# Performance work log

Measured on AMD Instinct MI355X. Metric: run time of the kernel, lower is better.

## Reference

```python
import jax, jax.numpy as jnp
import numpy as np

N_NODES = 25000
N_EDGES = 100000
N_GRAPHS = 1000
DIM = 64
NUM_FEAT = 14
EDGE_FEAT = 4
HIDDEN_EDGE = 128
NUM_OUT = 1
NUM_CONV_STEPS = 3
SET2SET_STEPS = 3
NEG_SLOPE = 0.01


def leaky_relu(x):
    return jnp.where(x > 0, x, NEG_SLOPE * x)


def setup_inputs() -> dict:
    key = jax.random.key(0)
    ks = jax.random.split(key, 24)
    s = lambda fan_in: 1.0 / np.sqrt(fan_in)
    inp = {
        "x": jax.random.normal(ks[0], (N_NODES, NUM_FEAT), dtype=jnp.float32),
        "edge_index": jax.random.randint(ks[1], (2, N_EDGES), 0, N_NODES),
        "edge_attr": jax.random.uniform(ks[2], (N_EDGES, EDGE_FEAT), dtype=jnp.float32),
        "batch": jnp.sort(jax.random.randint(ks[3], (N_NODES,), 0, N_GRAPHS)),
        # lin0
        "lin0_w": jax.random.normal(ks[4], (DIM, NUM_FEAT), dtype=jnp.float32) * s(NUM_FEAT),
        "lin0_b": jnp.zeros((DIM,), dtype=jnp.float32),
        # edge-weight MLP: Linear(4,128) -> LeakyReLU -> Linear(128, DIM*DIM)
        "net_w1": jax.random.normal(ks[5], (HIDDEN_EDGE, EDGE_FEAT), dtype=jnp.float32) * s(EDGE_FEAT),
        "net_b1": jnp.zeros((HIDDEN_EDGE,), dtype=jnp.float32),
        "net_w2": jax.random.normal(ks[6], (DIM * DIM, HIDDEN_EDGE), dtype=jnp.float32) * s(HIDDEN_EDGE),
        "net_b2": jnp.zeros((DIM * DIM,), dtype=jnp.float32),
        # NNConv root weight + bias
        "conv_root": jax.random.normal(ks[7], (DIM, DIM), dtype=jnp.float32) * s(DIM),
        "conv_bias": jnp.zeros((DIM,), dtype=jnp.float32),
        # GRU (single layer), torch gate order r,z,n
        "gru_w_ih": jax.random.normal(ks[8], (3 * DIM, DIM), dtype=jnp.float32) * s(DIM),
        "gru_w_hh": jax.random.normal(ks[9], (3 * DIM, DIM), dtype=jnp.float32) * s(DIM),
        "gru_b_ih": jnp.zeros((3 * DIM,), dtype=jnp.float32),
        "gru_b_hh": jnp.zeros((3 * DIM,), dtype=jnp.float32),
        # Set2Set LSTM: input 2*DIM -> hidden DIM, torch gate order i,f,g,o
        "lstm_w_ih": jax.random.normal(ks[10], (4 * DIM, 2 * DIM), dtype=jnp.float32) * s(2 * DIM),
        "lstm_w_hh": jax.random.normal(ks[11], (4 * DIM, DIM), dtype=jnp.float32) * s(DIM),
        "lstm_b_ih": jnp.zeros((4 * DIM,), dtype=jnp.float32),
        "lstm_b_hh": jnp.zeros((4 * DIM,), dtype=jnp.float32),
        # final linear on [B, 2*DIM]
        "lin_w": jax.random.normal(ks[12], (NUM_OUT, 2 * DIM), dtype=jnp.float32) * s(2 * DIM),
        "lin_b": jnp.zeros((NUM_OUT,), dtype=jnp.float32),
    }
    return inp


def _forward(x, edge_index, edge_attr, batch,
             lin0_w, lin0_b, net_w1, net_b1, net_w2, net_b2,
             conv_root, conv_bias, gru_w_ih, gru_w_hh, gru_b_ih, gru_b_hh,
             lstm_w_ih, lstm_w_hh, lstm_b_ih, lstm_b_hh, lin_w, lin_b):
    src, dst = edge_index[0], edge_index[1]

    out = leaky_relu(x @ lin0_w.T + lin0_b)          # [N, DIM]
    h = out                                          # GRU hidden [N, DIM]

    # edge_attr is constant across conv steps -> dynamic weights computed once
    W_e = (leaky_relu(edge_attr @ net_w1.T + net_b1) @ net_w2.T + net_b2)
    W_e = W_e.reshape(N_EDGES, DIM, DIM)             # [E, DIM, DIM]

    deg = jax.ops.segment_sum(jnp.ones((N_EDGES,), dtype=x.dtype), dst,
                              num_segments=N_NODES)
    inv_deg = jnp.where(deg > 0, 1.0 / jnp.maximum(deg, 1.0), 0.0)[:, None]

    for _ in range(NUM_CONV_STEPS):
        # NNConv: gather -> per-edge matmul -> scatter-mean, plus root term
        msg = jnp.einsum('ed,edo->eo', out[src], W_e)                 # [E, DIM]
        aggr = jax.ops.segment_sum(msg, dst, num_segments=N_NODES) * inv_deg
        m = leaky_relu(aggr + out @ conv_root + conv_bias)
        # single-step GRU (torch equations, gate order r,z,n)
        gi = m @ gru_w_ih.T + gru_b_ih
        gh = h @ gru_w_hh.T + gru_b_hh
        i_r, i_z, i_n = jnp.split(gi, 3, axis=-1)
        h_r, h_z, h_n = jnp.split(gh, 3, axis=-1)
        r = jax.nn.sigmoid(i_r + h_r)
        z = jax.nn.sigmoid(i_z + h_z)
        n = jnp.tanh(i_n + r * h_n)
        h = (1.0 - z) * n + z * h
        out = h

    # Set2Set pooling (processing_steps=3)
    q_star = jnp.zeros((N_GRAPHS, 2 * DIM), dtype=x.dtype)
    hl = jnp.zeros((N_GRAPHS, DIM), dtype=x.dtype)
    cl = jnp.zeros((N_GRAPHS, DIM), dtype=x.dtype)
    for _ in range(SET2SET_STEPS):
        gates = q_star @ lstm_w_ih.T + lstm_b_ih + hl @ lstm_w_hh.T + lstm_b_hh
        gi, gf, gg, go = jnp.split(gates, 4, axis=-1)
        cl = jax.nn.sigmoid(gf) * cl + jax.nn.sigmoid(gi) * jnp.tanh(gg)
        hl = jax.nn.sigmoid(go) * jnp.tanh(cl)
        q = hl                                                         # [B, DIM]
        e = jnp.sum(out * q[batch], axis=-1)                           # [N]
        e_max = jax.ops.segment_max(e, batch, num_segments=N_GRAPHS)
        e_exp = jnp.exp(e - e_max[batch])
        denom = jax.ops.segment_sum(e_exp, batch, num_segments=N_GRAPHS)
        a = e_exp / denom[batch]                                       # segment softmax
        r_read = jax.ops.segment_sum(a[:, None] * out, batch,
                                     num_segments=N_GRAPHS)            # [B, DIM]
        q_star = jnp.concatenate([q, r_read], axis=-1)

    return q_star @ lin_w.T + lin_b                                    # [B, NUM_OUT]


def reference(x, edge_index, edge_attr, batch,
              lin0_w, lin0_b, net_w1, net_b1, net_w2, net_b2,
              conv_root, conv_bias, gru_w_ih, gru_w_hh, gru_b_ih, gru_b_hh,
              lstm_w_ih, lstm_w_hh, lstm_b_ih, lstm_b_hh, lin_w, lin_b):
    return _forward(x, edge_index, edge_attr, batch,
                    lin0_w, lin0_b, net_w1, net_b1, net_w2, net_b2,
                    conv_root, conv_bias, gru_w_ih, gru_w_hh, gru_b_ih, gru_b_hh,
                    lstm_w_ih, lstm_w_hh, lstm_b_ih, lstm_b_hh, lin_w, lin_b)
```

## Files before the change

### kernel.cpp

```cpp
#include <hip/hip_runtime.h>
#include <math.h>

#define N_NODES_C  25000
#define N_EDGES_C  100000
#define N_GRAPHS_C 1000
#define EPB 128

typedef __attribute__((ext_vector_type(8))) _Float16 f16x8;
typedef __attribute__((ext_vector_type(2))) _Float16 f16x2;
typedef __attribute__((ext_vector_type(4))) float   f32x4;

__device__ __forceinline__ float lrelu(float x) { return x > 0.f ? x : 0.01f * x; }
__device__ __forceinline__ float sigm(float x)  { return 1.f / (1.f + __expf(-x)); }
__device__ __forceinline__ f32x4 MFH(f16x8 a, f16x8 b, f32x4 c) {
  return __builtin_amdgcn_mfma_f32_16x16x32_f16(a, b, c, 0, 0, 0);
}

__global__ __launch_bounds__(256) void lin0_kernel(const float* __restrict__ x,
                            const float* __restrict__ w, const float* __restrict__ b,
                            float* __restrict__ nodeF) {
  __shared__ float ws[64 * 15];
  __shared__ float bs[64];
  __shared__ float xr[4][16];
  const int tid = threadIdx.x;
  for (int i = tid; i < 896; i += 256) { int o = i / 14, j = i % 14; ws[o * 15 + j] = w[i]; }
  if (tid < 64) bs[tid] = b[tid];
  const int nl = tid >> 6, o = tid & 63;
  const int n = blockIdx.x * 4 + nl;
  if (o < 14 && n < N_NODES_C) xr[nl][o] = x[n * 14 + o];
  __syncthreads();
  if (n < N_NODES_C) {
    float s = bs[o];
#pragma unroll
    for (int j = 0; j < 14; ++j) s += xr[nl][j] * ws[o * 15 + j];
    nodeF[n * 64 + o] = lrelu(s);
  }
}

__global__ void deg_kernel(const int* __restrict__ ei, const int* __restrict__ batch,
                           float* __restrict__ deg, int* __restrict__ goff) {
  int e = blockIdx.x * blockDim.x + threadIdx.x;
  if (e < N_EDGES_C) atomicAdd(&deg[ei[N_EDGES_C + e]], 1.f);
  if (e <= N_GRAPHS_C) {
    int lo = 0, hi = N_NODES_C;
    while (lo < hi) { int mid = (lo + hi) >> 1; if (batch[mid] < e) lo = mid + 1; else hi = mid; }
    goff[e] = lo;
  }
}

__global__ void invdeg_kernel(float* __restrict__ deg) {
  int n = blockIdx.x * blockDim.x + threadIdx.x;
  if (n < N_NODES_C) { float v = deg[n]; deg[n] = v > 0.f ? 1.f / v : 0.f; }
}

__global__ __launch_bounds__(256) void prep_kernel(
    const float* __restrict__ net_w2, const float* __restrict__ net_b2,
    const float* __restrict__ conv_root,
    const float* __restrict__ w_ih, const float* __restrict__ w_hh,
    _Float16* __restrict__ Wp, _Float16* __restrict__ B2p,
    _Float16* __restrict__ Rtp, _Float16* __restrict__ Wip, _Float16* __restrict__ Whp) {
  int i = blockIdx.x * 256 + threadIdx.x;
  {
    int j = i & 7, lane = (i >> 3) & 63, q = (i >> 9) & 3, p = (i >> 11) & 1;
    int oh = (i >> 12) & 1, d = i >> 13;
    int kci = q >> 1, ob = q & 1;
    int col = lane & 15, kg = lane >> 4;
    int o = oh * 32 + ob * 16 + col, h = (p * 2 + kci) * 32 + kg * 8 + j;
    Wp[i] = (_Float16)net_w2[((size_t)d * 64 + o) * 128 + h];
  }
  if (i < 4096) {
    int j = i & 7, lane = (i >> 3) & 63, kc2 = (i >> 9) & 1, ob = (i >> 10) & 1, oh = (i >> 11) & 1;
    int col = lane & 15, kg = lane >> 4;
    int o = oh * 32 + ob * 16 + col, d = kc2 * 32 + kg * 8 + j;
    B2p[i] = (_Float16)net_b2[d * 64 + o];
  }
  if (i < 12288) {
    int j = i & 7, lane = (i >> 3) & 63, kc = (i >> 9) & 1, t = i >> 10;
    int o = t * 16 + (lane & 15), d = kc * 32 + (lane >> 4) * 8 + j;
    if (i < 4096) Rtp[i] = (_Float16)conv_root[d * 64 + o];
    Wip[i] = (_Float16)w_ih[o * 64 + d];
    Whp[i] = (_Float16)w_hh[o * 64 + d];
  }
}

__global__ __launch_bounds__(256, 3) void msg_kernel(
    const float* __restrict__ nodef,
    const int*   __restrict__ ei,
    const float* __restrict__ eattr,
    const float* __restrict__ net_w1,
    const float* __restrict__ net_b1,
    const _Float16* __restrict__ Wp,
    const _Float16* __restrict__ B2p,
    float* __restrict__ aggr)
{
  __shared__ _Float16 xsT[EPB * 64];
  __shared__ float    w1s[128 * 5];

  const int tid = threadIdx.x;
  const int e0 = blockIdx.x * EPB;

  if (tid < 128) {
    float4 wv = *(const float4*)(net_w1 + tid * 4);
    w1s[tid * 5 + 0] = wv.x; w1s[tid * 5 + 1] = wv.y;
    w1s[tid * 5 + 2] = wv.z; w1s[tid * 5 + 3] = wv.w;
    w1s[tid * 5 + 4] = net_b1[tid];
  }
  {
    const int e = tid >> 1, dh = (tid & 1) * 32;
    int ge = e0 + e;
    const int esw = (e & 7) << 3;
#pragma unroll
    for (int jb = 0; jb < 4; ++jb) {
      int d = dh + jb * 8;
      float4 v0, v1;
      if (ge < N_EDGES_C) {
        const float4* nf4 = (const float4*)(nodef + (size_t)ei[ge] * 64 + d);
        v0 = nf4[0]; v1 = nf4[1];
      } else {
        v0 = make_float4(0.f, 0.f, 0.f, 0.f); v1 = v0;
      }
      f16x8 pk;
      pk[0] = (_Float16)v0.x; pk[1] = (_Float16)v0.y; pk[2] = (_Float16)v0.z; pk[3] = (_Float16)v0.w;
      pk[4] = (_Float16)v1.x; pk[5] = (_Float16)v1.y; pk[6] = (_Float16)v1.z; pk[7] = (_Float16)v1.w;
      *(f16x8*)&xsT[e * 64 + (d ^ esw)] = pk;
    }
  }

  const int lane = tid & 63, wv = tid >> 6;
  const int e0w = (wv & 1) * 64;
  const int oh  = wv >> 1;
  const int col = lane & 15;
  const int kg  = lane >> 4;
  const int swz = (col & 7) << 3;

  __syncthreads();

  f32x4 acc[4][2];
#pragma unroll
  for (int eb = 0; eb < 4; ++eb) { acc[eb][0] = 0.f; acc[eb][1] = 0.f; }
#pragma unroll
  for (int ob = 0; ob < 2; ++ob)
#pragma unroll
    for (int kc2 = 0; kc2 < 2; ++kc2) {
      f16x8 b2f = *(const f16x8*)(B2p + oh * 2048 + ob * 1024 + kc2 * 512 + lane * 8);
#pragma unroll
      for (int eb = 0; eb < 4; ++eb) {
        f16x8 xf = *(const f16x8*)&xsT[(e0w + eb * 16 + col) * 64 + ((kc2 * 32 + kg * 8) ^ swz)];
        acc[eb][ob] = MFH(xf, b2f, acc[eb][ob]);
      }
    }

  float4 at[4];
#pragma unroll
  for (int eb = 0; eb < 4; ++eb) {
    int ge = e0 + e0w + eb * 16 + col;
    at[eb] = (ge < N_EDGES_C) ? *(const float4*)(eattr + (size_t)ge * 4)
                              : make_float4(0.f, 0.f, 0.f, 0.f);
  }

#define ISSUE(BUF, ADDR)                                                  \
  asm volatile("global_load_dwordx4 %0, %4, off\n\t"                      \
               "global_load_dwordx4 %1, %4, off offset:1024\n\t"          \
               "global_load_dwordx4 %2, %4, off offset:2048\n\t"          \
               "global_load_dwordx4 %3, %4, off offset:3072"              \
               : "=&v"(BUF[0]), "=&v"(BUF[1]), "=&v"(BUF[2]), "=&v"(BUF[3]) \
               : "v"(ADDR)                                                \
               : "memory")
#define COMPUTE(BUF, XV, J)                                               \
  {                                                                       \
    _Pragma("unroll")                                                     \
    for (int eb = 0; eb < 4; ++eb) {                                      \
      unsigned dw = XV[eb].u[(J) >> 1];                                   \
      unsigned xd = __builtin_amdgcn_perm(dw, dw, ((J) & 1) ? 0x03020302u : 0x01000100u); \
      f16x2 x2; { union { unsigned u; f16x2 h; } c; c.u = xd; x2 = c.h; } \
      _Pragma("unroll")                                                   \
      for (int kci = 0; kci < 2; ++kci) {                                 \
        union { f16x8 v; f16x2 pp[4]; } af, Uu;                           \
        af.v = Af[eb][kci];                                               \
        _Pragma("unroll")                                                 \
        for (int q = 0; q < 4; ++q) Uu.pp[q] = af.pp[q] * x2;             \
        acc[eb][0] = MFH(Uu.v, BUF[kci * 2 + 0], acc[eb][0]);             \
        acc[eb][1] = MFH(Uu.v, BUF[kci * 2 + 1], acc[eb][1]);             \
      }                                                                   \
    }                                                                     \
  }

  const _Float16* wp_base = Wp + oh * 4096 + lane * 8;
#pragma unroll 1
  for (int p = 0; p < 2; ++p) {
    f16x8 Af[4][2];
#pragma unroll
    for (int kci = 0; kci < 2; ++kci) {
      float4 wr[8]; float wb[8];
#pragma unroll
      for (int j = 0; j < 8; ++j) {
        int hq = (p * 2 + kci) * 32 + kg * 8 + j;
        wr[j] = *(const float4*)&w1s[hq * 5];
        wb[j] = w1s[hq * 5 + 4];
      }
#pragma unroll
      for (int eb = 0; eb < 4; ++eb) {
        f16x8 F;
#pragma unroll
        for (int j = 0; j < 8; ++j) {
          float a = wb[j] + at[eb].x * wr[j].x + at[eb].y * wr[j].y
                          + at[eb].z * wr[j].z + at[eb].w * wr[j].w;
          F[j] = (_Float16)lrelu(a);
        }
        Af[eb][kci] = F;
      }
    }

    const _Float16* wp_p = wp_base + p * 2048;
    f16x8 B0[4], B1[4];
    ISSUE(B0, wp_p);
    ISSUE(B1, wp_p + 8192);

#pragma unroll 1
    for (int d8 = 0; d8 < 64; d8 += 8) {
      union XU { f16x8 v; unsigned u[4]; };
      XU XV[4];
#pragma unroll
      for (int eb = 0; eb < 4; ++eb)
        XV[eb].v = *(const f16x8*)&xsT[(e0w + eb * 16 + col) * 64 + (d8 ^ swz)];
#pragma unroll
      for (int j = 0; j < 8; ++j) {
        const int d = d8 + j;
        if (d < 63) { asm volatile("s_waitcnt vmcnt(4)"); }
        else        { asm volatile("s_waitcnt vmcnt(0)"); }
        __builtin_amdgcn_sched_barrier(0);
        if ((j & 1) == 0) { COMPUTE(B0, XV, j); } else { COMPUTE(B1, XV, j); }
        __builtin_amdgcn_sched_barrier(0);
        if (d < 62) {
          const _Float16* adr = wp_p + (size_t)(d + 2) * 8192;
          if ((j & 1) == 0) { ISSUE(B0, adr); } else { ISSUE(B1, adr); }
        }
      }
    }
  }
#undef ISSUE
#undef COMPUTE

  const int o0w = oh * 32;
#pragma unroll
  for (int eb = 0; eb < 4; ++eb) {
#pragma unroll
    for (int r = 0; r < 4; ++r) {
      int e = e0w + eb * 16 + kg * 4 + r;
      int ge = e0 + e;
      if (ge < N_EDGES_C) {
        int dn = ei[N_EDGES_C + ge];
        atomicAdd(&aggr[(size_t)dn * 64 + o0w + col],      acc[eb][0][r]);
        atomicAdd(&aggr[(size_t)dn * 64 + o0w + 16 + col], acc[eb][1][r]);
      }
    }
  }
}

__global__ __launch_bounds__(128) void node_update_kernel(
    float* __restrict__ aggr, const float* __restrict__ invdeg,
    const _Float16* __restrict__ Rtp, const _Float16* __restrict__ Wip,
    const _Float16* __restrict__ Whp,
    const float* __restrict__ conv_bias,
    const float* __restrict__ b_ih, const float* __restrict__ b_hh,
    float* __restrict__ nodeF)
{
  __shared__ _Float16 ms[2][16 * 64];

  const int tid = threadIdx.x, lane = tid & 63, wv = tid >> 6;
  const int col = lane & 15, kg = lane >> 4;
  const int nwb = blockIdx.x * 32 + wv * 16;

  float invd[4]; int nrow[4];
#pragma unroll
  for (int r = 0; r < 4; ++r) {
    int nn = nwb + kg * 4 + r; nrow[r] = nn;
    invd[r] = (nn < N_NODES_C) ? invdeg[nn] : 0.f;
  }
  float ag[4][4];
#pragma unroll
  for (int t = 0; t < 4; ++t)
#pragma unroll
    for (int r = 0; r < 4; ++r) {
      int nn = nrow[r];
      ag[t][r] = (nn < N_NODES_C) ? aggr[(size_t)nn * 64 + t * 16 + col] : 0.f;
    }

  int arow = nwb + col; if (arow >= N_NODES_C) arow = N_NODES_C - 1;
  f16x8 nf[2];
#pragma unroll
  for (int kc = 0; kc < 2; ++kc) {
    f32x4 v0 = *(const f32x4*)(nodeF + (size_t)arow * 64 + kc * 32 + kg * 8);
    f32x4 v1 = *(const f32x4*)(nodeF + (size_t)arow * 64 + kc * 32 + kg * 8 + 4);
    f16x8 F;
#pragma unroll
    for (int j = 0; j < 4; ++j) { F[j] = (_Float16)v0[j]; F[4 + j] = (_Float16)v1[j]; }
    nf[kc] = F;
  }

  f32x4 racc[4];
#pragma unroll
  for (int t = 0; t < 4; ++t) racc[t] = conv_bias[t * 16 + col];
#pragma unroll
  for (int t = 0; t < 4; ++t)
#pragma unroll
    for (int kc = 0; kc < 2; ++kc)
      racc[t] = MFH(nf[kc], *(const f16x8*)(Rtp + t * 1024 + kc * 512 + lane * 8), racc[t]);

#pragma unroll
  for (int t = 0; t < 4; ++t) {
#pragma unroll
    for (int r = 0; r < 4; ++r) {
      int nn = nrow[r];
      if (nn < N_NODES_C) aggr[(size_t)nn * 64 + t * 16 + col] = 0.f;
      float mval = lrelu(ag[t][r] * invd[r] + racc[t][r]);
      int nl = kg * 4 + r;
      int dsw = (t * 16 + col) ^ ((nl & 7) << 3);
      ms[wv][nl * 64 + dsw] = (_Float16)mval;
    }
  }
  __syncthreads();

  f16x8 ma[2];
#pragma unroll
  for (int kc = 0; kc < 2; ++kc)
    ma[kc] = *(const f16x8*)&ms[wv][col * 64 + ((kc * 32 + kg * 8) ^ ((col & 7) << 3))];

  f32x4 gi[12], gh[12];
#pragma unroll
  for (int t = 0; t < 12; ++t) { gi[t] = b_ih[t * 16 + col]; gh[t] = b_hh[t * 16 + col]; }
#pragma unroll
  for (int t = 0; t < 12; ++t)
#pragma unroll
    for (int kc = 0; kc < 2; ++kc) {
      gi[t] = MFH(ma[kc], *(const f16x8*)(Wip + t * 1024 + kc * 512 + lane * 8), gi[t]);
      gh[t] = MFH(nf[kc], *(const f16x8*)(Whp + t * 1024 + kc * 512 + lane * 8), gh[t]);
    }

#pragma unroll
  for (int t = 0; t < 4; ++t) {
#pragma unroll
    for (int r = 0; r < 4; ++r) {
      int nn = nrow[r];
      if (nn >= N_NODES_C) continue;
      size_t idx = (size_t)nn * 64 + t * 16 + col;
      float hv = nodeF[idx];
      float rr = sigm(gi[t][r] + gh[t][r]);
      float zz = sigm(gi[t + 4][r] + gh[t + 4][r]);
      float nv = tanhf(gi[t + 8][r] + rr * gh[t + 8][r]);
      nodeF[idx] = (1.f - zz) * nv + zz * hv;
    }
  }
}

__global__ __launch_bounds__(256) void set2set_kernel(
    const float* __restrict__ nodeF, const int* __restrict__ goff,
    const float* __restrict__ w_ih, const float* __restrict__ w_hh,
    const float* __restrict__ b_ih, const float* __restrict__ b_hh,
    const float* __restrict__ lw, const float* __restrict__ lb,
    float* __restrict__ ebuf, float* __restrict__ dout)
{
  const int g = blockIdx.x, tid = threadIdx.x;
  const int t = tid & 63, grp = tid >> 6;
  __shared__ float qs[128], hs[64], cls[64], gvs[4][64], red[4][64], scal[8];
  if (tid < 128) qs[tid] = 0.f;
  if (tid < 64) { hs[tid] = 0.f; cls[tid] = 0.f; }
  const int s0 = goff[g], s1 = goff[g + 1];
  __syncthreads();

  for (int step = 0; step < 3; ++step) {
    {
      float s = b_ih[grp * 64 + t] + b_hh[grp * 64 + t];
      const float4* wi4 = (const float4*)(w_ih + (grp * 64 + t) * 128);
#pragma unroll 8
      for (int j = 0; j < 32; ++j) {
        float4 w = wi4[j];
        s += qs[4 * j] * w.x + qs[4 * j + 1] * w.y + qs[4 * j + 2] * w.z + qs[4 * j + 3] * w.w;
      }
      const float4* wh4 = (const float4*)(w_hh + (grp * 64 + t) * 64);
#pragma unroll 8
      for (int j = 0; j < 16; ++j) {
        float4 w = wh4[j];
        s += hs[4 * j] * w.x + hs[4 * j + 1] * w.y + hs[4 * j + 2] * w.z + hs[4 * j + 3] * w.w;
      }
      gvs[grp][t] = s;
    }
    __syncthreads();
    if (tid < 64) {
      float c = sigm(gvs[1][t]) * cls[t] + sigm(gvs[0][t]) * tanhf(gvs[2][t]);
      float hn = sigm(gvs[3][t]) * tanhf(c);
      cls[t] = c; hs[t] = hn; qs[t] = hn;
    }
    __syncthreads();
    const float qv = hs[t];

    float emax = -3.0e38f;
    for (int n = s0 + grp; n < s1; n += 4) {
      float p = nodeF[(size_t)n * 64 + t] * qv;
#pragma unroll
      for (int off = 32; off > 0; off >>= 1) p += __shfl_down(p, off);
      float en = __shfl(p, 0);
      if (t == 0) ebuf[n] = en;
      emax = fmaxf(emax, en);
    }
    if (t == 0) scal[grp] = emax;
    __syncthreads();
    emax = fmaxf(fmaxf(scal[0], scal[1]), fmaxf(scal[2], scal[3]));

    float lsum = 0.f;
    for (int n = s0 + tid; n < s1; n += 256) {
      float ex = __expf(ebuf[n] - emax);
      ebuf[n] = ex;
      lsum += ex;
    }
#pragma unroll
    for (int off = 32; off > 0; off >>= 1) lsum += __shfl_down(lsum, off);
    if (t == 0) scal[4 + grp] = lsum;
    __syncthreads();
    float denom = scal[4] + scal[5] + scal[6] + scal[7];

    float r = 0.f;
    for (int n = s0 + grp; n < s1; n += 4) r += ebuf[n] * nodeF[(size_t)n * 64 + t];
    red[grp][t] = r;
    __syncthreads();
    if (tid < 64) {
      float rr = red[0][t] + red[1][t] + red[2][t] + red[3][t];
      qs[64 + t] = (s1 > s0) ? rr / denom : 0.f;
    }
    __syncthreads();
  }
  float sacc = (tid < 128) ? qs[tid] * lw[tid] : 0.f;
#pragma unroll
  for (int off = 32; off > 0; off >>= 1) sacc += __shfl_down(sacc, off);
  if (t == 0) scal[grp] = sacc;
  __syncthreads();
  if (tid == 0) dout[g] = scal[0] + scal[1] + lb[0];
}

extern "C" void kernel_launch(void* const* d_in, const int* in_sizes, int n_in,
                              void* d_out, int out_size, void* d_ws, size_t ws_size,
                              hipStream_t stream) {
  const float* x         = (const float*)d_in[0];
  const int*   ei        = (const int*)  d_in[1];
  const float* eattr     = (const float*)d_in[2];
  const int*   batch     = (const int*)  d_in[3];
  const float* lin0_w    = (const float*)d_in[4];
  const float* lin0_b    = (const float*)d_in[5];
  const float* net_w1    = (const float*)d_in[6];
  const float* net_b1    = (const float*)d_in[7];
  const float* net_w2    = (const float*)d_in[8];
  const float* net_b2    = (const float*)d_in[9];
  const float* conv_root = (const float*)d_in[10];
  const float* conv_bias = (const float*)d_in[11];
  const float* gru_w_ih  = (const float*)d_in[12];
  const float* gru_w_hh  = (const float*)d_in[13];
  const float* gru_b_ih  = (const float*)d_in[14];
  const float* gru_b_hh  = (const float*)d_in[15];
  const float* lstm_w_ih = (const float*)d_in[16];
  const float* lstm_w_hh = (const float*)d_in[17];
  const float* lstm_b_ih = (const float*)d_in[18];
  const float* lstm_b_hh = (const float*)d_in[19];
  const float* lin_w     = (const float*)d_in[20];
  const float* lin_b     = (const float*)d_in[21];

  float* ws    = (float*)d_ws;
  float* nodeF = ws;
  float* aggr  = nodeF + 1600000;
  float* deg   = aggr + 1600000;
  float* ebuf  = deg + 25000;
  int*   goff  = (int*)(ebuf + 25000);
  _Float16* Rtp = (_Float16*)(goff + 1024);
  _Float16* Wip = Rtp + 4096;
  _Float16* Whp = Wip + 12288;
  _Float16* Wp  = Whp + 12288;
  _Float16* B2p = Wp + 524288;

  hipMemsetAsync(deg, 0, 25000 * sizeof(float), stream);
  hipMemsetAsync(aggr, 0, 1600000 * sizeof(float), stream);

  lin0_kernel<<<(N_NODES_C + 3) / 4, 256, 0, stream>>>(x, lin0_w, lin0_b, nodeF);
  deg_kernel<<<(N_EDGES_C + 255) / 256, 256, 0, stream>>>(ei, batch, deg, goff);
  invdeg_kernel<<<(N_NODES_C + 255) / 256, 256, 0, stream>>>(deg);
  prep_kernel<<<2048, 256, 0, stream>>>(net_w2, net_b2, conv_root, gru_w_ih, gru_w_hh,
                                        Wp, B2p, Rtp, Wip, Whp);

  for (int step = 0; step < 3; ++step) {
    msg_kernel<<<(N_EDGES_C + EPB - 1) / EPB, 256, 0, stream>>>(
        nodeF, ei, eattr, net_w1, net_b1, Wp, B2p, aggr);
    node_update_kernel<<<(N_NODES_C + 31) / 32, 128, 0, stream>>>(
        aggr, deg, Rtp, Wip, Whp, conv_bias, gru_b_ih, gru_b_hh, nodeF);
  }

  set2set_kernel<<<N_GRAPHS_C, 256, 0, stream>>>(
      nodeF, goff, lstm_w_ih, lstm_w_hh, lstm_b_ih, lstm_b_hh, lin_w, lin_b, ebuf, (float*)d_out);
}
```

Before: 564.6 us.

## Repartition msg kernel waves to cover all 64 outputs over 32 edges each

Each wave in the edge-message kernel now handles 32 edges and all 64 output columns, where before it handled 64 edges and half the outputs. The packed weight layout from prep_kernel is reordered to match, and each wave streams twice as many weight fragments per d step with a deeper vmcnt wait. The goal is to halve the per-wave edge-attribute MLP and A-fragment work that was duplicated across the two output halves. In exchange each wave loads twice as much Wp per edge tile from global memory and holds larger B buffers in registers, which may lower occupancy.

```diff
diff --git a/kernel.cpp b/kernel.cpp
--- a/kernel.cpp
+++ b/kernel.cpp
@@ -61,17 +61,16 @@
     _Float16* __restrict__ Rtp, _Float16* __restrict__ Wip, _Float16* __restrict__ Whp) {
   int i = blockIdx.x * 256 + threadIdx.x;
   {
-    int j = i & 7, lane = (i >> 3) & 63, q = (i >> 9) & 3, p = (i >> 11) & 1;
-    int oh = (i >> 12) & 1, d = i >> 13;
-    int kci = q >> 1, ob = q & 1;
+    int j = i & 7, lane = (i >> 3) & 63, obq = (i >> 9) & 3, kci = (i >> 11) & 1;
+    int p = (i >> 12) & 1, d = i >> 13;
     int col = lane & 15, kg = lane >> 4;
-    int o = oh * 32 + ob * 16 + col, h = (p * 2 + kci) * 32 + kg * 8 + j;
+    int o = obq * 16 + col, h = (p * 2 + kci) * 32 + kg * 8 + j;
     Wp[i] = (_Float16)net_w2[((size_t)d * 64 + o) * 128 + h];
   }
   if (i < 4096) {
-    int j = i & 7, lane = (i >> 3) & 63, kc2 = (i >> 9) & 1, ob = (i >> 10) & 1, oh = (i >> 11) & 1;
+    int j = i & 7, lane = (i >> 3) & 63, kc2 = (i >> 9) & 1, obq = (i >> 10) & 3;
     int col = lane & 15, kg = lane >> 4;
-    int o = oh * 32 + ob * 16 + col, d = kc2 * 32 + kg * 8 + j;
+    int o = obq * 16 + col, d = kc2 * 32 + kg * 8 + j;
     B2p[i] = (_Float16)net_b2[d * 64 + o];
   }
   if (i < 12288) {
@@ -127,32 +126,35 @@
   }
 
   const int lane = tid & 63, wv = tid >> 6;
-  const int e0w = (wv & 1) * 64;
-  const int oh  = wv >> 1;
+  const int e0w = wv * 32;
   const int col = lane & 15;
   const int kg  = lane >> 4;
   const int swz = (col & 7) << 3;
 
   __syncthreads();
 
-  f32x4 acc[4][2];
-#pragma unroll
-  for (int eb = 0; eb < 4; ++eb) { acc[eb][0] = 0.f; acc[eb][1] = 0.f; }
-#pragma unroll
-  for (int ob = 0; ob < 2; ++ob)
-#pragma unroll
-    for (int kc2 = 0; kc2 < 2; ++kc2) {
-      f16x8 b2f = *(const f16x8*)(B2p + oh * 2048 + ob * 1024 + kc2 * 512 + lane * 8);
-#pragma unroll
-      for (int eb = 0; eb < 4; ++eb) {
-        f16x8 xf = *(const f16x8*)&xsT[(e0w + eb * 16 + col) * 64 + ((kc2 * 32 + kg * 8) ^ swz)];
-        acc[eb][ob] = MFH(xf, b2f, acc[eb][ob]);
-      }
-    }
-
-  float4 at[4];
-#pragma unroll
-  for (int eb = 0; eb < 4; ++eb) {
+  f32x4 acc[2][4];
+#pragma unroll
+  for (int eb = 0; eb < 2; ++eb)
+#pragma unroll
+    for (int obq = 0; obq < 4; ++obq) acc[eb][obq] = 0.f;
+#pragma unroll
+  for (int kc2 = 0; kc2 < 2; ++kc2) {
+    f16x8 xf[2];
+#pragma unroll
+    for (int eb = 0; eb < 2; ++eb)
+      xf[eb] = *(const f16x8*)&xsT[(e0w + eb * 16 + col) * 64 + ((kc2 * 32 + kg * 8) ^ swz)];
+#pragma unroll
+    for (int obq = 0; obq < 4; ++obq) {
+      f16x8 b2f = *(const f16x8*)(B2p + (obq * 2 + kc2) * 512 + lane * 8);
+#pragma unroll
+      for (int eb = 0; eb < 2; ++eb) acc[eb][obq] = MFH(xf[eb], b2f, acc[eb][obq]);
+    }
+  }
+
+  float4 at[2];
+#pragma unroll
+  for (int eb = 0; eb < 2; ++eb) {
     int ge = e0 + e0w + eb * 16 + col;
     at[eb] = (ge < N_EDGES_C) ? *(const float4*)(eattr + (size_t)ge * 4)
                               : make_float4(0.f, 0.f, 0.f, 0.f);
@@ -163,13 +165,13 @@
                "global_load_dwordx4 %1, %4, off offset:1024\n\t"          \
                "global_load_dwordx4 %2, %4, off offset:2048\n\t"          \
                "global_load_dwordx4 %3, %4, off offset:3072"              \
-               : "=&v"(BUF[0]), "=&v"(BUF[1]), "=&v"(BUF[2]), "=&v"(BUF[3]) \
+               : "=&v"((BUF)[0]), "=&v"((BUF)[1]), "=&v"((BUF)[2]), "=&v"((BUF)[3]) \
                : "v"(ADDR)                                                \
                : "memory")
 #define COMPUTE(BUF, XV, J)                                               \
   {                                                                       \
     _Pragma("unroll")                                                     \
-    for (int eb = 0; eb < 4; ++eb) {                                      \
+    for (int eb = 0; eb < 2; ++eb) {                                      \
       unsigned dw = XV[eb].u[(J) >> 1];                                   \
       unsigned xd = __builtin_amdgcn_perm(dw, dw, ((J) & 1) ? 0x03020302u : 0x01000100u); \
       f16x2 x2; { union { unsigned u; f16x2 h; } c; c.u = xd; x2 = c.h; } \
@@ -179,16 +181,18 @@
         af.v = Af[eb][kci];                                               \
         _Pragma("unroll")                                                 \
         for (int q = 0; q < 4; ++q) Uu.pp[q] = af.pp[q] * x2;             \
-        acc[eb][0] = MFH(Uu.v, BUF[kci * 2 + 0], acc[eb][0]);             \
-        acc[eb][1] = MFH(Uu.v, BUF[kci * 2 + 1], acc[eb][1]);             \
+        acc[eb][0] = MFH(Uu.v, (BUF)[kci * 4 + 0], acc[eb][0]);           \
+        acc[eb][1] = MFH(Uu.v, (BUF)[kci * 4 + 1], acc[eb][1]);           \
+        acc[eb][2] = MFH(Uu.v, (BUF)[kci * 4 + 2], acc[eb][2]);           \
+        acc[eb][3] = MFH(Uu.v, (BUF)[kci * 4 + 3], acc[eb][3]);           \
       }                                                                   \
     }                                                                     \
   }
 
-  const _Float16* wp_base = Wp + oh * 4096 + lane * 8;
+  const _Float16* wp_base = Wp + lane * 8;
 #pragma unroll 1
   for (int p = 0; p < 2; ++p) {
-    f16x8 Af[4][2];
+    f16x8 Af[2][2];
 #pragma unroll
     for (int kci = 0; kci < 2; ++kci) {
       float4 wr[8]; float wb[8];
@@ -199,7 +203,7 @@
         wb[j] = w1s[hq * 5 + 4];
       }
 #pragma unroll
-      for (int eb = 0; eb < 4; ++eb) {
+      for (int eb = 0; eb < 2; ++eb) {
         f16x8 F;
 #pragma unroll
         for (int j = 0; j < 8; ++j) {
@@ -211,29 +215,32 @@
       }
     }
 
-    const _Float16* wp_p = wp_base + p * 2048;
-    f16x8 B0[4], B1[4];
-    ISSUE(B0, wp_p);
-    ISSUE(B1, wp_p + 8192);
+    const _Float16* wp_p = wp_base + p * 4096;
+    f16x8 B0[8], B1[8];
+    ISSUE(B0 + 0, wp_p);
+    ISSUE(B0 + 4, wp_p + 2048);
+    ISSUE(B1 + 0, wp_p + 8192);
+    ISSUE(B1 + 4, wp_p + 8192 + 2048);
 
 #pragma unroll 1
     for (int d8 = 0; d8 < 64; d8 += 8) {
       union XU { f16x8 v; unsigned u[4]; };
-      XU XV[4];
-#pragma unroll
-      for (int eb = 0; eb < 4; ++eb)
+      XU XV[2];
+#pragma unroll
+      for (int eb = 0; eb < 2; ++eb)
         XV[eb].v = *(const f16x8*)&xsT[(e0w + eb * 16 + col) * 64 + (d8 ^ swz)];
 #pragma unroll
       for (int j = 0; j < 8; ++j) {
         const int d = d8 + j;
-        if (d < 63) { asm volatile("s_waitcnt vmcnt(4)"); }
+        if (d < 63) { asm volatile("s_waitcnt vmcnt(8)"); }
         else        { asm volatile("s_waitcnt vmcnt(0)"); }
         __builtin_amdgcn_sched_barrier(0);
         if ((j & 1) == 0) { COMPUTE(B0, XV, j); } else { COMPUTE(B1, XV, j); }
         __builtin_amdgcn_sched_barrier(0);
         if (d < 62) {
           const _Float16* adr = wp_p + (size_t)(d + 2) * 8192;
-          if ((j & 1) == 0) { ISSUE(B0, adr); } else { ISSUE(B1, adr); }
+          if ((j & 1) == 0) { ISSUE(B0 + 0, adr); ISSUE(B0 + 4, adr + 2048); }
+          else              { ISSUE(B1 + 0, adr); ISSUE(B1 + 4, adr + 2048); }
         }
       }
     }
@@ -241,17 +248,17 @@
 #undef ISSUE
 #undef COMPUTE
 
-  const int o0w = oh * 32;
-#pragma unroll
-  for (int eb = 0; eb < 4; ++eb) {
+#pragma unroll
+  for (int eb = 0; eb < 2; ++eb) {
 #pragma unroll
     for (int r = 0; r < 4; ++r) {
       int e = e0w + eb * 16 + kg * 4 + r;
       int ge = e0 + e;
       if (ge < N_EDGES_C) {
         int dn = ei[N_EDGES_C + ge];
-        atomicAdd(&aggr[(size_t)dn * 64 + o0w + col],      acc[eb][0][r]);
-        atomicAdd(&aggr[(size_t)dn * 64 + o0w + 16 + col], acc[eb][1][r]);
+#pragma unroll
+        for (int obq = 0; obq < 4; ++obq)
+          atomicAdd(&aggr[(size_t)dn * 64 + obq * 16 + col], acc[eb][obq][r]);
       }
     }
   }
```

Measured after the change: 619.0 us. +9.6%, slower.
